# Kernel tuning notes

Hardware: AMD Instinct MI355X
Metric: run time of the kernel (lower is better)

## Reference

```python
import jax, jax.numpy as jnp
import numpy as np

B, S = 4, 512
IN_F, OUT_F, NUM_F = 1024, 512, 128


def setup_inputs() -> dict:
    key = jax.random.key(0)
    k1, k2, k3 = jax.random.split(key, 3)
    x = jax.random.normal(k1, (B, S, IN_F), dtype=jnp.float32)
    # xavier-uniform-style inits
    fb_bound = float(np.sqrt(6.0 / (IN_F + NUM_F)))
    feature_bank = jax.random.uniform(k2, (IN_F, NUM_F), dtype=jnp.float32,
                                      minval=-fb_bound, maxval=fb_bound)
    p_bound = float(np.sqrt(6.0 / (OUT_F + NUM_F)))
    prototypes = jax.random.uniform(k3, (OUT_F, NUM_F), dtype=jnp.float32,
                                    minval=-p_bound, maxval=p_bound)
    theta = jnp.float32(1.0)
    alpha = jnp.float32(0.5)
    beta = jnp.float32(0.5)
    return {"x": x, "feature_bank": feature_bank, "prototypes": prototypes,
            "theta": theta, "alpha": alpha, "beta": beta}


def reference(x, feature_bank, prototypes, theta, alpha, beta):
    # Project input onto feature bank: (B, S, NUM_F)
    a = jnp.einsum('bsi,if->bsf', x, feature_bank)
    a = a[..., None, :]            # (B, S, 1, NUM_F)
    b = prototypes                 # (OUT_F, NUM_F) broadcasts to (B, S, OUT_F, NUM_F)
    zero = jnp.zeros((), dtype=a.dtype)
    both = (a > 0) & (b > 0)
    # min-intersection over jointly-present features
    inter = jnp.sum(jnp.where(both, jnp.minimum(a, b), zero), axis=-1)
    # substract-match differences
    d_ab = jnp.sum(jnp.where(both & (a > b), a - b, zero), axis=-1)
    d_ba = jnp.sum(jnp.where(both & (b > a), b - a, zero), axis=-1)
    # contrast model
    return theta * inter - alpha * d_ab - beta * d_ba
```

## Files before the change

kernel.cpp:

```cpp
#include <hip/hip_runtime.h>


typedef __attribute__((ext_vector_type(8))) short s16x8;
typedef __attribute__((ext_vector_type(4))) float f32x4;

#define ROWS   2048
#define IN_F   1024
#define NUM_F  128
#define OUT_F  512

__device__ __forceinline__ unsigned short f2bf(float f) {
    unsigned u = __builtin_bit_cast(unsigned, f);
    return (unsigned short)((u + 0x7FFFu + ((u >> 16) & 1u)) >> 16);
}

__global__ __launch_bounds__(256) void k1_gemm_relu(const float* __restrict__ x,
                                                    const float* __restrict__ fb,
                                                    float2* __restrict__ up) {
    __shared__ unsigned short xs[16][136];
    __shared__ unsigned short fs[128][68];

    const int tid  = threadIdx.x;
    const int lane = tid & 63;
    const int w    = tid >> 6;
    const int bid  = blockIdx.x;
    const int fTile   = bid & 1;
    const int rowTile = bid >> 1;
    const int rowBase = rowTile * 16;
    const int n0      = fTile * 64;

    const int srow = tid >> 4;
    const int scol = tid & 15;

    f32x4 acc = {0.f, 0.f, 0.f, 0.f};

    for (int kc = 0; kc < 8; ++kc) {
        const int k0 = kc * 128;
        {
            const float* gx = x + (size_t)(rowBase + srow) * IN_F + k0 + scol * 8;
            float4 v0 = *(const float4*)gx;
            float4 v1 = *(const float4*)(gx + 4);
            s16x8 h;
            h[0] = (short)f2bf(v0.x); h[1] = (short)f2bf(v0.y);
            h[2] = (short)f2bf(v0.z); h[3] = (short)f2bf(v0.w);
            h[4] = (short)f2bf(v1.x); h[5] = (short)f2bf(v1.y);
            h[6] = (short)f2bf(v1.z); h[7] = (short)f2bf(v1.w);
            *(s16x8*)&xs[srow][scol * 8] = h;
        }
        #pragma unroll
        for (int jj = 0; jj < 8; ++jj) {
            const int kk = srow + 16 * jj;
            float4 v = *(const float4*)(fb + (size_t)(k0 + kk) * NUM_F + n0 + scol * 4);
            ushort4 h;
            h.x = f2bf(v.x); h.y = f2bf(v.y); h.z = f2bf(v.z); h.w = f2bf(v.w);
            *(ushort4*)&fs[kk][scol * 4] = h;
        }
        __syncthreads();

        #pragma unroll
        for (int ks = 0; ks < 4; ++ks) {
            const int kb = ks * 32 + (lane >> 4) * 8;
            s16x8 a = *(const s16x8*)&xs[lane & 15][kb];
            s16x8 b;
            const int nn = w * 16 + (lane & 15);
            #pragma unroll
            for (int i = 0; i < 8; ++i) b[i] = (short)fs[kb + i][nn];
            acc = __builtin_amdgcn_mfma_f32_16x16x32_bf16(a, b, acc, 0, 0, 0);
        }
        __syncthreads();
    }

    const int col   = lane & 15;
    const int rbase = (lane >> 4) * 4;
    #pragma unroll
    for (int r = 0; r < 4; ++r) {
        const float c   = acc[r];
        const int   row = rowBase + rbase + r;
        const int   f   = n0 + w * 16 + col;
        up[(size_t)row * NUM_F + f] = make_float2(fmaxf(c, 0.f), c > 0.f ? 1.f : 0.f);
    }
}

__global__ __launch_bounds__(256) void k2_tversky(const float2* __restrict__ up,
                                                  const float* __restrict__ prot,
                                                  const float* __restrict__ thp,
                                                  const float* __restrict__ alp,
                                                  const float* __restrict__ bep,
                                                  float* __restrict__ out) {
    __shared__ float2 us[64][34];
    __shared__ float2 vs[64][34];

    const int tid = threadIdx.x;
    const int tc  = tid & 15;
    const int tr  = tid >> 4;
    const int bid = blockIdx.x;
    const int colBase = (bid & 7) * 64;
    const int rowBase = (bid >> 3) * 64;

    float sm[4][4] = {{0.f}};
    float sa[4][4] = {{0.f}};
    float sp[4][4] = {{0.f}};

    for (int c = 0; c < 4; ++c) {
        const int f0 = c * 32;
        #pragma unroll
        for (int t = 0; t < 4; ++t) {
            const int li  = tid + 256 * t;
            const int row = li >> 4;
            const int p4  = li & 15;
            float4 v = *(const float4*)((const float*)up +
                        ((size_t)(rowBase + row) * NUM_F + f0) * 2 + p4 * 4);
            *(float4*)&us[row][p4 * 2] = v;
        }
        #pragma unroll
        for (int t = 0; t < 2; ++t) {
            const int li  = tid + 256 * t;
            const int row = li >> 3;
            const int q   = li & 7;
            float4 v = *(const float4*)(prot + (size_t)(colBase + row) * NUM_F + f0 + q * 4);
            float4 w0 = make_float4(fmaxf(v.x, 0.f), v.x > 0.f ? 1.f : 0.f,
                                    fmaxf(v.y, 0.f), v.y > 0.f ? 1.f : 0.f);
            float4 w1 = make_float4(fmaxf(v.z, 0.f), v.z > 0.f ? 1.f : 0.f,
                                    fmaxf(v.w, 0.f), v.w > 0.f ? 1.f : 0.f);
            *(float4*)&vs[row][q * 4]     = w0;
            *(float4*)&vs[row][q * 4 + 2] = w1;
        }
        __syncthreads();

        #pragma unroll 2
        for (int kk = 0; kk < 32; ++kk) {
            float2 uu[4], vv[4];
            #pragma unroll
            for (int i = 0; i < 4; ++i) uu[i] = us[tr + 16 * i][kk];
            #pragma unroll
            for (int j = 0; j < 4; ++j) vv[j] = vs[tc + 16 * j][kk];
            #pragma unroll
            for (int i = 0; i < 4; ++i) {
                #pragma unroll
                for (int j = 0; j < 4; ++j) {
                    sm[i][j] += fminf(uu[i].x, vv[j].x);
                    sa[i][j] += uu[i].x * vv[j].y;
                    sp[i][j] += vv[j].x * uu[i].y;
                }
            }
        }
        __syncthreads();
    }

    const float th = *thp, al = *alp, be = *bep;
    const float c0 = th + al + be;
    #pragma unroll
    for (int i = 0; i < 4; ++i) {
        #pragma unroll
        for (int j = 0; j < 4; ++j) {
            out[(size_t)(rowBase + tr + 16 * i) * OUT_F + colBase + tc + 16 * j] =
                c0 * sm[i][j] - al * sa[i][j] - be * sp[i][j];
        }
    }
}

extern "C" void kernel_launch(void* const* d_in, const int* in_sizes, int n_in,
                              void* d_out, int out_size, void* d_ws, size_t ws_size,
                              hipStream_t stream) {
    const float* x    = (const float*)d_in[0];
    const float* fb   = (const float*)d_in[1];
    const float* prot = (const float*)d_in[2];
    const float* thp  = (const float*)d_in[3];
    const float* alp  = (const float*)d_in[4];
    const float* bep  = (const float*)d_in[5];
    float* out = (float*)d_out;
    float2* up = (float2*)d_ws;

    k1_gemm_relu<<<256, 256, 0, stream>>>(x, fb, up);
    k2_tversky<<<256, 256, 0, stream>>>(up, prot, thp, alp, bep, out);
}
```

Measured before the change: 100.6 us.

## Move Tversky difference sums onto bf16 MFMA and pre-transpose feature bank

```diff
diff --git a/kernel.cpp b/kernel.cpp
--- a/kernel.cpp
+++ b/kernel.cpp
@@ -3,31 +3,87 @@
 
 typedef __attribute__((ext_vector_type(8))) short s16x8;
 typedef __attribute__((ext_vector_type(4))) float f32x4;
+typedef unsigned short u16;
 
 #define ROWS   2048
 #define IN_F   1024
 #define NUM_F  128
 #define OUT_F  512
 
-__device__ __forceinline__ unsigned short f2bf(float f) {
+__device__ __forceinline__ u16 f2bf(float f) {
     unsigned u = __builtin_bit_cast(unsigned, f);
-    return (unsigned short)((u + 0x7FFFu + ((u >> 16) & 1u)) >> 16);
+    return (u16)((u + 0x7FFFu + ((u >> 16) & 1u)) >> 16);
+}
+__device__ __forceinline__ float bfu(u16 h) {
+    return __builtin_bit_cast(float, (unsigned)h << 16);
+}
+
+#define UBF_OFF   0
+#define SUBF_OFF  (2048*128)
+#define VBF_OFF   (2*2048*128)
+#define SVBF_OFF  (2*2048*128 + 512*128)
+#define FBT_OFF   (2*2048*128 + 2*512*128)
+
+__global__ __launch_bounds__(256) void k0_convert(const float* __restrict__ fb,
+                                                  const float* __restrict__ prot,
+                                                  u16* __restrict__ ws) {
+    const int tid = threadIdx.x;
+    const int b   = blockIdx.x;
+    if (b < 32) {
+        __shared__ u16 tr[64][72];
+        const int kt = b >> 1, ft = b & 1;
+        #pragma unroll
+        for (int t = 0; t < 4; ++t) {
+            const int li = tid + 256 * t;
+            const int kl = li >> 4;
+            const int f4 = li & 15;
+            float4 v = *(const float4*)(fb + (size_t)(kt * 64 + kl) * NUM_F + ft * 64 + f4 * 4);
+            tr[f4 * 4 + 0][kl] = f2bf(v.x);
+            tr[f4 * 4 + 1][kl] = f2bf(v.y);
+            tr[f4 * 4 + 2][kl] = f2bf(v.z);
+            tr[f4 * 4 + 3][kl] = f2bf(v.w);
+        }
+        __syncthreads();
+        u16* fbT = ws + FBT_OFF;
+        const int fl = tid >> 2;
+        const int kq = tid & 3;
+        s16x8 a0 = *(const s16x8*)&tr[fl][kq * 16];
+        s16x8 a1 = *(const s16x8*)&tr[fl][kq * 16 + 8];
+        u16* dst = fbT + (size_t)(ft * 64 + fl) * IN_F + kt * 64 + kq * 16;
+        *(s16x8*)dst       = a0;
+        *(s16x8*)(dst + 8) = a1;
+    } else {
+        const int pb = b - 32;
+        u16* vbf  = ws + VBF_OFF;
+        u16* svbf = ws + SVBF_OFF;
+        #pragma unroll
+        for (int t = 0; t < 8; ++t) {
+            const int i4 = pb * 2048 + tid + 256 * t;
+            float4 p = ((const float4*)prot)[i4];
+            ushort4 vv, sv;
+            vv.x = f2bf(fmaxf(p.x, 0.f)); sv.x = p.x > 0.f ? 0x3F80 : 0;
+            vv.y = f2bf(fmaxf(p.y, 0.f)); sv.y = p.y > 0.f ? 0x3F80 : 0;
+            vv.z = f2bf(fmaxf(p.z, 0.f)); sv.z = p.z > 0.f ? 0x3F80 : 0;
+            vv.w = f2bf(fmaxf(p.w, 0.f)); sv.w = p.w > 0.f ? 0x3F80 : 0;
+            ((ushort4*)vbf)[i4]  = vv;
+            ((ushort4*)svbf)[i4] = sv;
+        }
+    }
 }
 
 __global__ __launch_bounds__(256) void k1_gemm_relu(const float* __restrict__ x,
-                                                    const float* __restrict__ fb,
-                                                    float2* __restrict__ up) {
-    __shared__ unsigned short xs[16][136];
-    __shared__ unsigned short fs[128][68];
+                                                    u16* __restrict__ ws) {
+    __shared__ u16 xs[16][136];
+    __shared__ u16 fsT[64][136];
+    const u16* fbT = ws + FBT_OFF;
+    u16* ubf  = ws + UBF_OFF;
+    u16* subf = ws + SUBF_OFF;
 
     const int tid  = threadIdx.x;
     const int lane = tid & 63;
     const int w    = tid >> 6;
-    const int bid  = blockIdx.x;
-    const int fTile   = bid & 1;
-    const int rowTile = bid >> 1;
-    const int rowBase = rowTile * 16;
-    const int n0      = fTile * 64;
+    const int rowBase = (blockIdx.x >> 1) * 16;
+    const int n0      = (blockIdx.x & 1) * 64;
 
     const int srow = tid >> 4;
     const int scol = tid & 15;
@@ -48,12 +104,12 @@
             *(s16x8*)&xs[srow][scol * 8] = h;
         }
         #pragma unroll
-        for (int jj = 0; jj < 8; ++jj) {
-            const int kk = srow + 16 * jj;
-            float4 v = *(const float4*)(fb + (size_t)(k0 + kk) * NUM_F + n0 + scol * 4);
-            ushort4 h;
-            h.x = f2bf(v.x); h.y = f2bf(v.y); h.z = f2bf(v.z); h.w = f2bf(v.w);
-            *(ushort4*)&fs[kk][scol * 4] = h;
+        for (int t = 0; t < 4; ++t) {
+            const int li  = tid + 256 * t;
+            const int row = li >> 4;
+            const int s8  = li & 15;
+            *(s16x8*)&fsT[row][s8 * 8] =
+                *(const s16x8*)(fbT + (size_t)(n0 + row) * IN_F + k0 + s8 * 8);
         }
         __syncthreads();
 
@@ -61,10 +117,7 @@
         for (int ks = 0; ks < 4; ++ks) {
             const int kb = ks * 32 + (lane >> 4) * 8;
             s16x8 a = *(const s16x8*)&xs[lane & 15][kb];
-            s16x8 b;
-            const int nn = w * 16 + (lane & 15);
-            #pragma unroll
-            for (int i = 0; i < 8; ++i) b[i] = (short)fs[kb + i][nn];
+            s16x8 b = *(const s16x8*)&fsT[w * 16 + (lane & 15)][kb];
             acc = __builtin_amdgcn_mfma_f32_16x16x32_bf16(a, b, acc, 0, 0, 0);
         }
         __syncthreads();
@@ -77,84 +130,116 @@
         const float c   = acc[r];
         const int   row = rowBase + rbase + r;
         const int   f   = n0 + w * 16 + col;
-        up[(size_t)row * NUM_F + f] = make_float2(fmaxf(c, 0.f), c > 0.f ? 1.f : 0.f);
-    }
-}
-
-__global__ __launch_bounds__(256) void k2_tversky(const float2* __restrict__ up,
-                                                  const float* __restrict__ prot,
+        ubf [(size_t)row * NUM_F + f] = f2bf(fmaxf(c, 0.f));
+        subf[(size_t)row * NUM_F + f] = c > 0.f ? 0x3F80 : 0;
+    }
+}
+
+__global__ __launch_bounds__(256) void k2_tversky(const u16* __restrict__ ws,
                                                   const float* __restrict__ thp,
                                                   const float* __restrict__ alp,
                                                   const float* __restrict__ bep,
                                                   float* __restrict__ out) {
-    __shared__ float2 us[64][34];
-    __shared__ float2 vs[64][34];
-
-    const int tid = threadIdx.x;
-    const int tc  = tid & 15;
-    const int tr  = tid >> 4;
-    const int bid = blockIdx.x;
-    const int colBase = (bid & 7) * 64;
-    const int rowBase = (bid >> 3) * 64;
-
-    float sm[4][4] = {{0.f}};
-    float sa[4][4] = {{0.f}};
-    float sp[4][4] = {{0.f}};
-
-    for (int c = 0; c < 4; ++c) {
-        const int f0 = c * 32;
-        #pragma unroll
-        for (int t = 0; t < 4; ++t) {
-            const int li  = tid + 256 * t;
-            const int row = li >> 4;
-            const int p4  = li & 15;
-            float4 v = *(const float4*)((const float*)up +
-                        ((size_t)(rowBase + row) * NUM_F + f0) * 2 + p4 * 4);
-            *(float4*)&us[row][p4 * 2] = v;
-        }
-        #pragma unroll
-        for (int t = 0; t < 2; ++t) {
-            const int li  = tid + 256 * t;
-            const int row = li >> 3;
-            const int q   = li & 7;
-            float4 v = *(const float4*)(prot + (size_t)(colBase + row) * NUM_F + f0 + q * 4);
-            float4 w0 = make_float4(fmaxf(v.x, 0.f), v.x > 0.f ? 1.f : 0.f,
-                                    fmaxf(v.y, 0.f), v.y > 0.f ? 1.f : 0.f);
-            float4 w1 = make_float4(fmaxf(v.z, 0.f), v.z > 0.f ? 1.f : 0.f,
-                                    fmaxf(v.w, 0.f), v.w > 0.f ? 1.f : 0.f);
-            *(float4*)&vs[row][q * 4]     = w0;
-            *(float4*)&vs[row][q * 4 + 2] = w1;
-        }
-        __syncthreads();
-
-        #pragma unroll 2
-        for (int kk = 0; kk < 32; ++kk) {
-            float2 uu[4], vv[4];
-            #pragma unroll
-            for (int i = 0; i < 4; ++i) uu[i] = us[tr + 16 * i][kk];
-            #pragma unroll
-            for (int j = 0; j < 4; ++j) vv[j] = vs[tc + 16 * j][kk];
-            #pragma unroll
-            for (int i = 0; i < 4; ++i) {
-                #pragma unroll
-                for (int j = 0; j < 4; ++j) {
-                    sm[i][j] += fminf(uu[i].x, vv[j].x);
-                    sa[i][j] += uu[i].x * vv[j].y;
-                    sp[i][j] += vv[j].x * uu[i].y;
-                }
-            }
-        }
-        __syncthreads();
+    __shared__ u16 us[32][136];
+    __shared__ u16 ss[32][136];
+    __shared__ u16 vs[64][136];
+    __shared__ u16 ps[64][136];
+    __shared__ float comb[32][68];
+
+    const u16* ubf  = ws + UBF_OFF;
+    const u16* subf = ws + SUBF_OFF;
+    const u16* vbf  = ws + VBF_OFF;
+    const u16* svbf = ws + SVBF_OFF;
+
+    const int tid  = threadIdx.x;
+    const int lane = tid & 63;
+    const int w    = tid >> 6;
+    const int tc   = tid & 15;
+    const int tr   = (tid >> 4) & 15;
+    const int rowBase = (blockIdx.x >> 3) * 32;
+    const int colBase = (blockIdx.x & 7) * 64;
+
+    #pragma unroll
+    for (int t = 0; t < 2; ++t) {
+        const int li  = tid + 256 * t;
+        const int row = li >> 4;
+        const int s8  = li & 15;
+        *(s16x8*)&us[row][s8 * 8] = *(const s16x8*)(ubf  + (size_t)(rowBase + row) * NUM_F + s8 * 8);
+        *(s16x8*)&ss[row][s8 * 8] = *(const s16x8*)(subf + (size_t)(rowBase + row) * NUM_F + s8 * 8);
+    }
+    #pragma unroll
+    for (int t = 0; t < 4; ++t) {
+        const int li  = tid + 256 * t;
+        const int row = li >> 4;
+        const int s8  = li & 15;
+        *(s16x8*)&vs[row][s8 * 8] = *(const s16x8*)(vbf  + (size_t)(colBase + row) * NUM_F + s8 * 8);
+        *(s16x8*)&ps[row][s8 * 8] = *(const s16x8*)(svbf + (size_t)(colBase + row) * NUM_F + s8 * 8);
+    }
+    __syncthreads();
+
+    const int rowOff = (w >> 1) * 16;
+    const int colOff = (w & 1) * 32;
+    f32x4 asa[2] = {{0,0,0,0},{0,0,0,0}};
+    f32x4 asp[2] = {{0,0,0,0},{0,0,0,0}};
+    #pragma unroll
+    for (int ks = 0; ks < 4; ++ks) {
+        const int kb = ks * 32 + (lane >> 4) * 8;
+        s16x8 au = *(const s16x8*)&us[rowOff + (lane & 15)][kb];
+        s16x8 as = *(const s16x8*)&ss[rowOff + (lane & 15)][kb];
+        #pragma unroll
+        for (int nt = 0; nt < 2; ++nt) {
+            s16x8 bv = *(const s16x8*)&vs[colOff + nt * 16 + (lane & 15)][kb];
+            s16x8 bs = *(const s16x8*)&ps[colOff + nt * 16 + (lane & 15)][kb];
+            asa[nt] = __builtin_amdgcn_mfma_f32_16x16x32_bf16(au, bs, asa[nt], 0, 0, 0);
+            asp[nt] = __builtin_amdgcn_mfma_f32_16x16x32_bf16(as, bv, asp[nt], 0, 0, 0);
+        }
+    }
+
+    float sm[2][4] = {{0.f}};
+    #pragma unroll 4
+    for (int g = 0; g < 16; ++g) {
+        s16x8 U0 = *(const s16x8*)&us[tr][g * 8];
+        s16x8 U1 = *(const s16x8*)&us[tr + 16][g * 8];
+        s16x8 V0 = *(const s16x8*)&vs[tc][g * 8];
+        s16x8 V1 = *(const s16x8*)&vs[tc + 16][g * 8];
+        s16x8 V2 = *(const s16x8*)&vs[tc + 32][g * 8];
+        s16x8 V3 = *(const s16x8*)&vs[tc + 48][g * 8];
+        #pragma unroll
+        for (int e = 0; e < 8; ++e) {
+            const float u0 = bfu((u16)U0[e]);
+            const float u1 = bfu((u16)U1[e]);
+            const float v0 = bfu((u16)V0[e]);
+            const float v1 = bfu((u16)V1[e]);
+            const float v2 = bfu((u16)V2[e]);
+            const float v3 = bfu((u16)V3[e]);
+            sm[0][0] += fminf(u0, v0); sm[0][1] += fminf(u0, v1);
+            sm[0][2] += fminf(u0, v2); sm[0][3] += fminf(u0, v3);
+            sm[1][0] += fminf(u1, v0); sm[1][1] += fminf(u1, v1);
+            sm[1][2] += fminf(u1, v2); sm[1][3] += fminf(u1, v3);
+        }
     }
 
     const float th = *thp, al = *alp, be = *bep;
     const float c0 = th + al + be;
-    #pragma unroll
-    for (int i = 0; i < 4; ++i) {
+
+    __syncthreads();
+    #pragma unroll
+    for (int nt = 0; nt < 2; ++nt) {
+        #pragma unroll
+        for (int r = 0; r < 4; ++r) {
+            const int row = rowOff + (lane >> 4) * 4 + r;
+            const int cp  = colOff + nt * 16 + (lane & 15);
+            comb[row][cp] = al * asa[nt][r] + be * asp[nt][r];
+        }
+    }
+    __syncthreads();
+
+    #pragma unroll
+    for (int i = 0; i < 2; ++i) {
         #pragma unroll
         for (int j = 0; j < 4; ++j) {
             out[(size_t)(rowBase + tr + 16 * i) * OUT_F + colBase + tc + 16 * j] =
-                c0 * sm[i][j] - al * sa[i][j] - be * sp[i][j];
+                c0 * sm[i][j] - comb[tr + 16 * i][tc + 16 * j];
         }
     }
 }
@@ -169,8 +254,9 @@
     const float* alp  = (const float*)d_in[4];
     const float* bep  = (const float*)d_in[5];
     float* out = (float*)d_out;
-    float2* up = (float2*)d_ws;
-
-    k1_gemm_relu<<<256, 256, 0, stream>>>(x, fb, up);
-    k2_tversky<<<256, 256, 0, stream>>>(up, prot, thp, alp, bep, out);
-}
+    u16*   ws  = (u16*)d_ws;
+
+    k0_convert  <<<40,  256, 0, stream>>>(fb, prot, ws);
+    k1_gemm_relu<<<256, 256, 0, stream>>>(x, ws);
+    k2_tversky  <<<512, 256, 0, stream>>>(ws, thp, alp, bep, out);
+}
```

Measured after the change: 92.45 us. -8.1%, faster.

## Offload Tversky product terms to fp16 MFMA and use packed fp16 min

Applied to the files above, without the earlier changes.

```diff
diff --git a/kernel.cpp b/kernel.cpp
--- a/kernel.cpp
+++ b/kernel.cpp
@@ -1,34 +1,59 @@
 #include <hip/hip_runtime.h>
 
 
-typedef __attribute__((ext_vector_type(8))) short s16x8;
-typedef __attribute__((ext_vector_type(4))) float f32x4;
+typedef _Float16 f16;
+typedef __attribute__((ext_vector_type(8))) _Float16 f16x8;
+typedef __attribute__((ext_vector_type(4))) _Float16 f16x4;
+typedef __attribute__((ext_vector_type(4))) float    f32x4;
 
 #define ROWS   2048
 #define IN_F   1024
 #define NUM_F  128
 #define OUT_F  512
 
-__device__ __forceinline__ unsigned short f2bf(float f) {
-    unsigned u = __builtin_bit_cast(unsigned, f);
-    return (unsigned short)((u + 0x7FFFu + ((u >> 16) & 1u)) >> 16);
-}
-
-__global__ __launch_bounds__(256) void k1_gemm_relu(const float* __restrict__ x,
-                                                    const float* __restrict__ fb,
-                                                    float2* __restrict__ up) {
-    __shared__ unsigned short xs[16][136];
-    __shared__ unsigned short fs[128][68];
+#define UH_OFF  0
+#define FBT_OFF (ROWS * NUM_F)
+
+__global__ __launch_bounds__(256) void k0_fbT(const float* __restrict__ fb,
+                                              f16* __restrict__ ws) {
+    __shared__ f16 tr[64][72];
+    const int tid = threadIdx.x;
+    const int kt  = blockIdx.x >> 1;
+    const int ft  = blockIdx.x & 1;
+    #pragma unroll
+    for (int t = 0; t < 4; ++t) {
+        const int li = tid + 256 * t;
+        const int kl = li >> 4;
+        const int f4 = li & 15;
+        float4 v = *(const float4*)(fb + (size_t)(kt * 64 + kl) * NUM_F + ft * 64 + f4 * 4);
+        tr[f4 * 4 + 0][kl] = (f16)v.x;
+        tr[f4 * 4 + 1][kl] = (f16)v.y;
+        tr[f4 * 4 + 2][kl] = (f16)v.z;
+        tr[f4 * 4 + 3][kl] = (f16)v.w;
+    }
+    __syncthreads();
+    f16* fbT = ws + FBT_OFF;
+    const int fl = tid >> 2;
+    const int kq = tid & 3;
+    f16x8 a0 = *(const f16x8*)&tr[fl][kq * 16];
+    f16x8 a1 = *(const f16x8*)&tr[fl][kq * 16 + 8];
+    f16* dst = fbT + (size_t)(ft * 64 + fl) * IN_F + kt * 64 + kq * 16;
+    *(f16x8*)dst       = a0;
+    *(f16x8*)(dst + 8) = a1;
+}
+
+__global__ __launch_bounds__(256) void k1_gemm(const float* __restrict__ x,
+                                               f16* __restrict__ ws) {
+    __shared__ f16 xs[16][136];
+    __shared__ f16 fsT[64][136];
+    const f16* fbT = ws + FBT_OFF;
+    f16* UH = ws + UH_OFF;
 
     const int tid  = threadIdx.x;
     const int lane = tid & 63;
     const int w    = tid >> 6;
-    const int bid  = blockIdx.x;
-    const int fTile   = bid & 1;
-    const int rowTile = bid >> 1;
-    const int rowBase = rowTile * 16;
-    const int n0      = fTile * 64;
-
+    const int rowBase = (blockIdx.x >> 1) * 16;
+    const int n0      = (blockIdx.x & 1) * 64;
     const int srow = tid >> 4;
     const int scol = tid & 15;
 
@@ -40,32 +65,27 @@
             const float* gx = x + (size_t)(rowBase + srow) * IN_F + k0 + scol * 8;
             float4 v0 = *(const float4*)gx;
             float4 v1 = *(const float4*)(gx + 4);
-            s16x8 h;
-            h[0] = (short)f2bf(v0.x); h[1] = (short)f2bf(v0.y);
-            h[2] = (short)f2bf(v0.z); h[3] = (short)f2bf(v0.w);
-            h[4] = (short)f2bf(v1.x); h[5] = (short)f2bf(v1.y);
-            h[6] = (short)f2bf(v1.z); h[7] = (short)f2bf(v1.w);
-            *(s16x8*)&xs[srow][scol * 8] = h;
-        }
-        #pragma unroll
-        for (int jj = 0; jj < 8; ++jj) {
-            const int kk = srow + 16 * jj;
-            float4 v = *(const float4*)(fb + (size_t)(k0 + kk) * NUM_F + n0 + scol * 4);
-            ushort4 h;
-            h.x = f2bf(v.x); h.y = f2bf(v.y); h.z = f2bf(v.z); h.w = f2bf(v.w);
-            *(ushort4*)&fs[kk][scol * 4] = h;
+            f16x8 h;
+            h[0] = (f16)v0.x; h[1] = (f16)v0.y; h[2] = (f16)v0.z; h[3] = (f16)v0.w;
+            h[4] = (f16)v1.x; h[5] = (f16)v1.y; h[6] = (f16)v1.z; h[7] = (f16)v1.w;
+            *(f16x8*)&xs[srow][scol * 8] = h;
+        }
+        #pragma unroll
+        for (int t = 0; t < 4; ++t) {
+            const int li  = tid + 256 * t;
+            const int row = li >> 4;
+            const int s8  = li & 15;
+            *(f16x8*)&fsT[row][s8 * 8] =
+                *(const f16x8*)(fbT + (size_t)(n0 + row) * IN_F + k0 + s8 * 8);
         }
         __syncthreads();
 
         #pragma unroll
         for (int ks = 0; ks < 4; ++ks) {
             const int kb = ks * 32 + (lane >> 4) * 8;
-            s16x8 a = *(const s16x8*)&xs[lane & 15][kb];
-            s16x8 b;
-            const int nn = w * 16 + (lane & 15);
-            #pragma unroll
-            for (int i = 0; i < 8; ++i) b[i] = (short)fs[kb + i][nn];
-            acc = __builtin_amdgcn_mfma_f32_16x16x32_bf16(a, b, acc, 0, 0, 0);
+            f16x8 a = *(const f16x8*)&xs[lane & 15][kb];
+            f16x8 b = *(const f16x8*)&fsT[w * 16 + (lane & 15)][kb];
+            acc = __builtin_amdgcn_mfma_f32_16x16x32_f16(a, b, acc, 0, 0, 0);
         }
         __syncthreads();
     }
@@ -77,84 +97,121 @@
         const float c   = acc[r];
         const int   row = rowBase + rbase + r;
         const int   f   = n0 + w * 16 + col;
-        up[(size_t)row * NUM_F + f] = make_float2(fmaxf(c, 0.f), c > 0.f ? 1.f : 0.f);
-    }
-}
-
-__global__ __launch_bounds__(256) void k2_tversky(const float2* __restrict__ up,
+        UH[(size_t)row * NUM_F + f] = (f16)fmaxf(c, 0.f);
+    }
+}
+
+__global__ __launch_bounds__(256) void k2_tversky(const f16* __restrict__ ws,
                                                   const float* __restrict__ prot,
                                                   const float* __restrict__ thp,
                                                   const float* __restrict__ alp,
                                                   const float* __restrict__ bep,
                                                   float* __restrict__ out) {
-    __shared__ float2 us[64][34];
-    __shared__ float2 vs[64][34];
-
-    const int tid = threadIdx.x;
-    const int tc  = tid & 15;
-    const int tr  = tid >> 4;
-    const int bid = blockIdx.x;
-    const int colBase = (bid & 7) * 64;
-    const int rowBase = (bid >> 3) * 64;
-
-    float sm[4][4] = {{0.f}};
-    float sa[4][4] = {{0.f}};
-    float sp[4][4] = {{0.f}};
-
-    for (int c = 0; c < 4; ++c) {
-        const int f0 = c * 32;
-        #pragma unroll
-        for (int t = 0; t < 4; ++t) {
-            const int li  = tid + 256 * t;
-            const int row = li >> 4;
-            const int p4  = li & 15;
-            float4 v = *(const float4*)((const float*)up +
-                        ((size_t)(rowBase + row) * NUM_F + f0) * 2 + p4 * 4);
-            *(float4*)&us[row][p4 * 2] = v;
-        }
-        #pragma unroll
-        for (int t = 0; t < 2; ++t) {
-            const int li  = tid + 256 * t;
-            const int row = li >> 3;
-            const int q   = li & 7;
-            float4 v = *(const float4*)(prot + (size_t)(colBase + row) * NUM_F + f0 + q * 4);
-            float4 w0 = make_float4(fmaxf(v.x, 0.f), v.x > 0.f ? 1.f : 0.f,
-                                    fmaxf(v.y, 0.f), v.y > 0.f ? 1.f : 0.f);
-            float4 w1 = make_float4(fmaxf(v.z, 0.f), v.z > 0.f ? 1.f : 0.f,
-                                    fmaxf(v.w, 0.f), v.w > 0.f ? 1.f : 0.f);
-            *(float4*)&vs[row][q * 4]     = w0;
-            *(float4*)&vs[row][q * 4 + 2] = w1;
-        }
-        __syncthreads();
-
-        #pragma unroll 2
-        for (int kk = 0; kk < 32; ++kk) {
-            float2 uu[4], vv[4];
+    __shared__ __align__(16) char smem[2 * 64 * 136 * 2];
+    f16 (*us)[136] = (f16(*)[136])smem;
+    f16 (*vs)[136] = (f16(*)[136])(smem + 64 * 136 * 2);
+
+    const f16* UH = ws + UH_OFF;
+
+    const int tid  = threadIdx.x;
+    const int lane = tid & 63;
+    const int w    = tid >> 6;
+    const int rowBase = (blockIdx.x >> 3) * 64;
+    const int colBase = (blockIdx.x & 7) * 64;
+
+    #pragma unroll
+    for (int t = 0; t < 4; ++t) {
+        const int li  = tid + 256 * t;
+        const int row = li >> 4;
+        const int s8  = li & 15;
+        *(f16x8*)&us[row][s8 * 8] = *(const f16x8*)(UH + (size_t)(rowBase + row) * NUM_F + s8 * 8);
+    }
+    #pragma unroll
+    for (int t = 0; t < 8; ++t) {
+        const int li  = tid + 256 * t;
+        const int row = li >> 5;
+        const int q   = li & 31;
+        float4 p = *(const float4*)(prot + (size_t)(colBase + row) * NUM_F + q * 4);
+        f16x4 v;
+        v[0] = (f16)fmaxf(p.x, 0.f); v[1] = (f16)fmaxf(p.y, 0.f);
+        v[2] = (f16)fmaxf(p.z, 0.f); v[3] = (f16)fmaxf(p.w, 0.f);
+        *(f16x4*)&vs[row][q * 4] = v;
+    }
+    __syncthreads();
+
+    const int rowOff = w * 16;
+    f32x4 asa[4], asp[4];
+    #pragma unroll
+    for (int nt = 0; nt < 4; ++nt) {
+        asa[nt] = (f32x4){0.f, 0.f, 0.f, 0.f};
+        asp[nt] = (f32x4){0.f, 0.f, 0.f, 0.f};
+    }
+    #pragma unroll
+    for (int ks = 0; ks < 4; ++ks) {
+        const int kb = ks * 32 + (lane >> 4) * 8;
+        f16x8 au = *(const f16x8*)&us[rowOff + (lane & 15)][kb];
+        f16x8 as_;
+        #pragma unroll
+        for (int e = 0; e < 8; ++e) as_[e] = au[e] > (f16)0 ? (f16)1 : (f16)0;
+        #pragma unroll
+        for (int nt = 0; nt < 4; ++nt) {
+            f16x8 bv = *(const f16x8*)&vs[nt * 16 + (lane & 15)][kb];
+            f16x8 bs;
             #pragma unroll
-            for (int i = 0; i < 4; ++i) uu[i] = us[tr + 16 * i][kk];
+            for (int e = 0; e < 8; ++e) bs[e] = bv[e] > (f16)0 ? (f16)1 : (f16)0;
+            asa[nt] = __builtin_amdgcn_mfma_f32_16x16x32_f16(au, bs, asa[nt], 0, 0, 0);
+            asp[nt] = __builtin_amdgcn_mfma_f32_16x16x32_f16(as_, bv, asp[nt], 0, 0, 0);
+        }
+    }
+
+    const int tr = tid >> 4;
+    const int tc = tid & 15;
+    f16x8 acc[4][4];
+    #pragma unroll
+    for (int i = 0; i < 4; ++i)
+        #pragma unroll
+        for (int j = 0; j < 4; ++j)
+            acc[i][j] = (f16x8){0, 0, 0, 0, 0, 0, 0, 0};
+
+    #pragma unroll
+    for (int g = 0; g < 16; ++g) {
+        f16x8 U[4], V[4];
+        #pragma unroll
+        for (int i = 0; i < 4; ++i) U[i] = *(const f16x8*)&us[tr + 16 * i][g * 8];
+        #pragma unroll
+        for (int j = 0; j < 4; ++j) V[j] = *(const f16x8*)&vs[tc + 16 * j][g * 8];
+        #pragma unroll
+        for (int i = 0; i < 4; ++i)
             #pragma unroll
-            for (int j = 0; j < 4; ++j) vv[j] = vs[tc + 16 * j][kk];
-            #pragma unroll
-            for (int i = 0; i < 4; ++i) {
-                #pragma unroll
-                for (int j = 0; j < 4; ++j) {
-                    sm[i][j] += fminf(uu[i].x, vv[j].x);
-                    sa[i][j] += uu[i].x * vv[j].y;
-                    sp[i][j] += vv[j].x * uu[i].y;
-                }
-            }
-        }
-        __syncthreads();
+            for (int j = 0; j < 4; ++j)
+                acc[i][j] += __builtin_elementwise_min(U[i], V[j]);
     }
 
     const float th = *thp, al = *alp, be = *bep;
     const float c0 = th + al + be;
+
+    __syncthreads();
+    float (*comb)[68] = (float(*)[68])smem;
+    #pragma unroll
+    for (int nt = 0; nt < 4; ++nt) {
+        #pragma unroll
+        for (int r = 0; r < 4; ++r) {
+            const int row = rowOff + (lane >> 4) * 4 + r;
+            const int cp  = nt * 16 + (lane & 15);
+            comb[row][cp] = al * asa[nt][r] + be * asp[nt][r];
+        }
+    }
+    __syncthreads();
+
     #pragma unroll
     for (int i = 0; i < 4; ++i) {
         #pragma unroll
         for (int j = 0; j < 4; ++j) {
+            float s = 0.f;
+            #pragma unroll
+            for (int e = 0; e < 8; ++e) s += (float)acc[i][j][e];
             out[(size_t)(rowBase + tr + 16 * i) * OUT_F + colBase + tc + 16 * j] =
-                c0 * sm[i][j] - al * sa[i][j] - be * sp[i][j];
+                c0 * s - comb[tr + 16 * i][tc + 16 * j];
         }
     }
 }
@@ -169,8 +226,9 @@
     const float* alp  = (const float*)d_in[4];
     const float* bep  = (const float*)d_in[5];
     float* out = (float*)d_out;
-    float2* up = (float2*)d_ws;
-
-    k1_gemm_relu<<<256, 256, 0, stream>>>(x, fb, up);
-    k2_tversky<<<256, 256, 0, stream>>>(up, prot, thp, alp, bep, out);
-}
+    f16*   ws  = (f16*)d_ws;
+
+    k0_fbT    <<<32,  256, 0, stream>>>(fb, ws);
+    k1_gemm   <<<256, 256, 0, stream>>>(x, ws);
+    k2_tversky<<<256, 256, 0, stream>>>(ws, prot, thp, alp, bep, out);
+}
```

Measured after the change: 87.53 us. -13.0%, faster.
